# Optimization experiments

Measured on AMD Instinct MI355X. Metric: run time of the kernel, lower is better.

## Reference

```python
import jax, jax.numpy as jnp
import numpy as np

T = 200000


def _sine_layer(tvec, A, w, phi, phic, wc):
    # tvec: (t,), A/w/phi: (n,1), phic/wc: (1,)
    phi_static = jax.nn.relu(phic)  # (1,)
    w_static = jax.nn.relu(wc)
    ph = jax.nn.relu(phi) + phi_static  # (n,1)
    ww = jax.nn.relu(w) + w_static
    sine = A * jnp.sin(ww * tvec[None, :] + ph)  # (n,t)
    return sine, phi_static, w_static


def _selector_layer(tvec, wave_input, w, phi, phic, wc, phi_prev, w_prev):
    # wave_input: (n,t), w/phi: (m,n), phic/wc/phi_prev/w_prev: (1,)
    # NOTE: phi_prev/w_prev passed but phi_prev flag is False in the network,
    # so they are NOT added (matches torch: `if self.phi_prev and ...`).
    phi_static = jax.nn.relu(phic)
    w_static = jax.nn.relu(wc)
    ph = (jax.nn.relu(phi) + phi_static)[:, :, None]  # (m,n,1)
    ww = (jax.nn.relu(w) + w_static)[:, :, None]
    sine = 0.5 * jnp.sin(ww * tvec[None, None, :] + ph) + 0.5  # (m,n,t)
    out = jnp.einsum('mnt,nt->mt', sine, wave_input)  # (m,t)
    return out, phi_static, w_static


def setup_inputs() -> dict:
    key = jax.random.key(0)
    ks = jax.random.split(key, 18)
    r = lambda k, s: jax.random.normal(k, s, dtype=jnp.float32)
    return {
        'initial_wave_input': r(ks[0], (20, T)),
        'A0': r(ks[1], (20, 1)), 'w0': r(ks[2], (20, 1)), 'phi0': r(ks[3], (20, 1)),
        'wc0': r(ks[4], (1,)), 'phic0': r(ks[5], (1,)),
        'w1': r(ks[6], (25, 20)), 'phi1': r(ks[7], (25, 20)),
        'wc1': r(ks[8], (1,)), 'phic1': r(ks[9], (1,)),
        'w2': r(ks[10], (30, 25)), 'phi2': r(ks[11], (30, 25)),
        'wc2': r(ks[12], (1,)), 'phic2': r(ks[13], (1,)),
        'w3': r(ks[14], (1, 30)), 'phi3': r(ks[15], (1, 30)),
        'wc3': r(ks[16], (1,)), 'phic3': r(ks[17], (1,)),
    }


def reference(initial_wave_input, A0, w0, phi0, wc0, phic0,
              w1, phi1, wc1, phic1, w2, phi2, wc2, phic2,
              w3, phi3, wc3, phic3):
    tvec = jnp.linspace(1.0, 1000.0, T, dtype=jnp.float32)
    # initial_wave_input is an argument of the torch module but is never used.
    s, phi, w = _sine_layer(tvec, A0, w0, phi0, phic0, wc0)
    s, phi, w = _selector_layer(tvec, s, w1, phi1, phic1, wc1, phi, w)
    s, phi, w = _selector_layer(tvec, s, w2, phi2, phic2, wc2, phi, w)
    s, phi, w = _selector_layer(tvec, s, w3, phi3, phic3, wc3, phi, w)
    return s  # (1, t)
```

## Files before the change

### kernel.cpp

```cpp
#include <hip/hip_runtime.h>
#include <hip/hip_bf16.h>

#define T_TOTAL 200000

typedef float v4f __attribute__((ext_vector_type(4)));

__device__ float g_P[4496];

__device__ __forceinline__ float sinp(float rev) {
    float g = __builtin_amdgcn_fractf(rev);
    float h = g - 0.5f;
    float u = h * h;
    float p = fmaf(45.621248f, u, -82.391040f);
    p = fmaf(p, u, 64.671616f);
    p = fmaf(p, u, -19.730960f);
    p = fmaf(p, u, 0.9999618f);
    return p;
}

__global__ void prep_kernel(
    const float* __restrict__ A0,
    const float* __restrict__ w0, const float* __restrict__ phi0,
    const float* __restrict__ wc0, const float* __restrict__ phic0,
    const float* __restrict__ w1, const float* __restrict__ phi1,
    const float* __restrict__ wc1, const float* __restrict__ phic1,
    const float* __restrict__ w2, const float* __restrict__ phi2,
    const float* __restrict__ wc2, const float* __restrict__ phic2,
    const float* __restrict__ w3, const float* __restrict__ phi3,
    const float* __restrict__ wc3, const float* __restrict__ phic3)
{
    const int tid = blockIdx.x * blockDim.x + threadIdx.x;
    const int stride = blockDim.x * gridDim.x;

    const double I2PI = 0.15915494309189535;
    const double D64  = 64.0 * 999.0 / 199999.0;

    const double ws0 = fmax((double)wc0[0], 0.0), ps0 = fmax((double)phic0[0], 0.0);
    const double ws1 = fmax((double)wc1[0], 0.0), ps1 = fmax((double)phic1[0], 0.0);
    const double ws2 = fmax((double)wc2[0], 0.0), ps2 = fmax((double)phic2[0], 0.0);
    const double ws3 = fmax((double)wc3[0], 0.0), ps3 = fmax((double)phic3[0], 0.0);

    for (int n = tid; n < 20; n += stride) {
        double wr = fmax((double)w0[n], 0.0) + ws0;
        g_P[n]      = (float)(wr * I2PI);
        g_P[20 + n] = (float)((fmax((double)phi0[n], 0.0) + ps0) * I2PI + 0.25);
        g_P[40 + n] = (float)(2.0 * cos(wr * D64));
        g_P[60 + n] = A0[n];
    }
    for (int k = tid; k < 20 * 32; k += stride) {
        const int n = k >> 5, m = k & 31;
        float wwf = 0.0f, phf = 0.25f, cf = 2.0f;
        if (m < 25) {
            const int s = m * 20 + n;
            double wr = fmax((double)w1[s], 0.0) + ws1;
            wwf = (float)(wr * I2PI);
            phf = (float)((fmax((double)phi1[s], 0.0) + ps1) * I2PI + 0.25);
            cf  = (float)(2.0 * cos(wr * D64));
        }
        g_P[80 + 96 * n + m]      = wwf;
        g_P[80 + 96 * n + 32 + m] = phf;
        g_P[80 + 96 * n + 64 + m] = cf;
    }
    for (int k = tid; k < 25 * 32; k += stride) {
        const int n = k >> 5, m = k & 31;
        float wwf = 0.0f, phf = 0.25f, cf = 2.0f;
        if (m < 30) {
            const int s = m * 25 + n;
            double wr = fmax((double)w2[s], 0.0) + ws2;
            wwf = (float)(wr * I2PI);
            phf = (float)((fmax((double)phi2[s], 0.0) + ps2) * I2PI + 0.25);
            cf  = (float)(2.0 * cos(wr * D64));
        }
        g_P[2000 + 96 * n + m]      = wwf;
        g_P[2000 + 96 * n + 32 + m] = phf;
        g_P[2000 + 96 * n + 64 + m] = cf;
    }
    for (int k = tid; k < 32; k += stride) {
        float wwf = 0.0f, phf = 0.0f, cf = 2.0f;
        if (k < 30) {
            double wr = fmax((double)w3[k], 0.0) + ws3;
            wwf = (float)(wr * I2PI);
            phf = (float)((fmax((double)phi3[k], 0.0) + ps3) * I2PI + 0.25);
            cf  = (float)(2.0 * cos(wr * D64));
        }
        g_P[4400 + k]      = wwf;
        g_P[4400 + 32 + k] = phf;
        g_P[4400 + 64 + k] = cf;
    }
}

__launch_bounds__(256)
__global__ void wave_main(float* __restrict__ out)
{
    __shared__ float sh0[20][64][4];
    __shared__ float sh1[25][64][4];
    __shared__ float shp[4][64][4];

    const int l = threadIdx.x & 63;
    const int w = __builtin_amdgcn_readfirstlane(threadIdx.x >> 6);
    const int tb = blockIdx.x * 256;
    const float STEP = 999.0f / 199999.0f;

    float tv[4];
#pragma unroll
    for (int j = 0; j < 4; ++j)
        tv[j] = fmaf((float)(tb + l + 64 * j), STEP, 1.0f);

#pragma unroll
    for (int i = 0; i < 5; ++i) {
        const int n = 5 * w + i;
        const float ww = g_P[n], ph = g_P[20 + n], C = g_P[40 + n], A = g_P[60 + n];
        float x0 = A * sinp(fmaf(ww, tv[0], ph));
        float x1 = A * sinp(fmaf(ww, tv[1], ph));
        float x2 = fmaf(C, x1, -x0);
        float x3 = fmaf(C, x2, -x1);
        *(v4f*)&sh0[n][l][0] = (v4f){x0, x1, x2, x3};
    }
    __syncthreads();

    float acc1[8][4] = {};
    float sum0[4] = {0.f, 0.f, 0.f, 0.f};
#pragma clang loop unroll(disable)
    for (int n = 0; n < 20; ++n) {
        const v4f s0 = *(const v4f*)&sh0[n][l][0];
#pragma unroll
        for (int j = 0; j < 4; ++j) sum0[j] += s0[j];
        const float* __restrict__ pb = &g_P[80 + 96 * n + 8 * w];
#pragma unroll
        for (int k = 0; k < 8; ++k) {
            const float ww = pb[k], ph = pb[32 + k], C = pb[64 + k];
            float x0 = sinp(fmaf(ww, tv[0], ph));
            float x1 = sinp(fmaf(ww, tv[1], ph));
            float x2 = fmaf(C, x1, -x0);
            float x3 = fmaf(C, x2, -x1);
            acc1[k][0] = fmaf(x0, s0[0], acc1[k][0]);
            acc1[k][1] = fmaf(x1, s0[1], acc1[k][1]);
            acc1[k][2] = fmaf(x2, s0[2], acc1[k][2]);
            acc1[k][3] = fmaf(x3, s0[3], acc1[k][3]);
        }
    }
#pragma unroll
    for (int k = 0; k < 8; ++k) {
        if (8 * w + k < 25) {
            v4f v;
#pragma unroll
            for (int j = 0; j < 4; ++j) v[j] = fmaf(0.5f, acc1[k][j], 0.5f * sum0[j]);
            *(v4f*)&sh1[8 * w + k][l][0] = v;
        }
    }
    __syncthreads();

    float acc2[8][4] = {};
    float sum1[4] = {0.f, 0.f, 0.f, 0.f};
#pragma clang loop unroll(disable)
    for (int n = 0; n < 25; ++n) {
        const v4f s1 = *(const v4f*)&sh1[n][l][0];
#pragma unroll
        for (int j = 0; j < 4; ++j) sum1[j] += s1[j];
        const float* __restrict__ pb = &g_P[2000 + 96 * n + 8 * w];
#pragma unroll
        for (int k = 0; k < 8; ++k) {
            const float ww = pb[k], ph = pb[32 + k], C = pb[64 + k];
            float x0 = sinp(fmaf(ww, tv[0], ph));
            float x1 = sinp(fmaf(ww, tv[1], ph));
            float x2 = fmaf(C, x1, -x0);
            float x3 = fmaf(C, x2, -x1);
            acc2[k][0] = fmaf(x0, s1[0], acc2[k][0]);
            acc2[k][1] = fmaf(x1, s1[1], acc2[k][1]);
            acc2[k][2] = fmaf(x2, s1[2], acc2[k][2]);
            acc2[k][3] = fmaf(x3, s1[3], acc2[k][3]);
        }
    }
    float s2r[8][4];
#pragma unroll
    for (int k = 0; k < 8; ++k)
#pragma unroll
        for (int j = 0; j < 4; ++j)
            s2r[k][j] = fmaf(0.5f, acc2[k][j], 0.5f * sum1[j]);

    float pw[4] = {0.f, 0.f, 0.f, 0.f};
    {
        const float* __restrict__ pb = &g_P[4400 + 8 * w];
#pragma unroll
        for (int k = 0; k < 8; ++k) {
            if (8 * w + k < 30) {
                const float ww = pb[k], ph = pb[32 + k], C = pb[64 + k];
                float x0 = sinp(fmaf(ww, tv[0], ph));
                float x1 = sinp(fmaf(ww, tv[1], ph));
                float x2 = fmaf(C, x1, -x0);
                float x3 = fmaf(C, x2, -x1);
                pw[0] = fmaf(fmaf(0.5f, x0, 0.5f), s2r[k][0], pw[0]);
                pw[1] = fmaf(fmaf(0.5f, x1, 0.5f), s2r[k][1], pw[1]);
                pw[2] = fmaf(fmaf(0.5f, x2, 0.5f), s2r[k][2], pw[2]);
                pw[3] = fmaf(fmaf(0.5f, x3, 0.5f), s2r[k][3], pw[3]);
            }
        }
    }
    *(v4f*)&shp[w][l][0] = (v4f){pw[0], pw[1], pw[2], pw[3]};
    __syncthreads();

    const float r = (shp[0][l][w] + shp[1][l][w]) + (shp[2][l][w] + shp[3][l][w]);
    const int tt = tb + l + 64 * w;
    if (tt < T_TOTAL) out[tt] = r;
}

extern "C" void kernel_launch(void* const* d_in, const int* in_sizes, int n_in,
                              void* d_out, int out_size, void* d_ws, size_t ws_size,
                              hipStream_t stream) {
    (void)in_sizes; (void)n_in; (void)d_ws; (void)ws_size; (void)out_size;
    const float* A0    = (const float*)d_in[1];
    const float* w0    = (const float*)d_in[2];
    const float* phi0  = (const float*)d_in[3];
    const float* wc0   = (const float*)d_in[4];
    const float* phic0 = (const float*)d_in[5];
    const float* w1    = (const float*)d_in[6];
    const float* phi1  = (const float*)d_in[7];
    const float* wc1   = (const float*)d_in[8];
    const float* phic1 = (const float*)d_in[9];
    const float* w2    = (const float*)d_in[10];
    const float* phi2  = (const float*)d_in[11];
    const float* wc2   = (const float*)d_in[12];
    const float* phic2 = (const float*)d_in[13];
    const float* w3    = (const float*)d_in[14];
    const float* phi3  = (const float*)d_in[15];
    const float* wc3   = (const float*)d_in[16];
    const float* phic3 = (const float*)d_in[17];

    float* out = (float*)d_out;

    hipLaunchKernelGGL(prep_kernel, dim3(6), dim3(256), 0, stream,
                       A0, w0, phi0, wc0, phic0,
                       w1, phi1, wc1, phic1,
                       w2, phi2, wc2, phic2,
                       w3, phi3, wc3, phic3);

    const int grid = (T_TOTAL + 255) / 256;
    hipLaunchKernelGGL(wave_main, dim3(grid), dim3(256), 0, stream, out);
}
```

Before: 54.69 us.

## Split selector output channels across eight wavefronts per block instead of four

Doubles the block to 512 threads so each wavefront handles 4 output channels per selector layer instead of 8, while each block still covers 256 time points. The parameter table is padded to 24 layer-0 entries so each of the 8 waves computes 3 input waves. Shared memory is overlaid so the partial-sum buffer reuses the first buffer, which needs an extra barrier, and the final reduction sums 8 partials per point. The aim is to cut per-thread register pressure and serial work and so raise occupancy. The cost is that the shared s0/s1 loads and their running sums are now repeated across twice as many waves.

```diff
diff --git a/kernel.cpp b/kernel.cpp
--- a/kernel.cpp
+++ b/kernel.cpp
@@ -5,7 +5,7 @@
 
 typedef float v4f __attribute__((ext_vector_type(4)));
 
-__device__ float g_P[4496];
+__device__ float g_P[4512];
 
 __device__ __forceinline__ float sinp(float rev) {
     float g = __builtin_amdgcn_fractf(rev);
@@ -40,12 +40,19 @@
     const double ws2 = fmax((double)wc2[0], 0.0), ps2 = fmax((double)phic2[0], 0.0);
     const double ws3 = fmax((double)wc3[0], 0.0), ps3 = fmax((double)phic3[0], 0.0);
 
-    for (int n = tid; n < 20; n += stride) {
-        double wr = fmax((double)w0[n], 0.0) + ws0;
-        g_P[n]      = (float)(wr * I2PI);
-        g_P[20 + n] = (float)((fmax((double)phi0[n], 0.0) + ps0) * I2PI + 0.25);
-        g_P[40 + n] = (float)(2.0 * cos(wr * D64));
-        g_P[60 + n] = A0[n];
+    for (int n = tid; n < 24; n += stride) {
+        float wwf = 0.0f, phf = 0.25f, cf = 2.0f, af = 0.0f;
+        if (n < 20) {
+            double wr = fmax((double)w0[n], 0.0) + ws0;
+            wwf = (float)(wr * I2PI);
+            phf = (float)((fmax((double)phi0[n], 0.0) + ps0) * I2PI + 0.25);
+            cf  = (float)(2.0 * cos(wr * D64));
+            af  = A0[n];
+        }
+        g_P[n]      = wwf;
+        g_P[24 + n] = phf;
+        g_P[48 + n] = cf;
+        g_P[72 + n] = af;
     }
     for (int k = tid; k < 20 * 32; k += stride) {
         const int n = k >> 5, m = k & 31;
@@ -57,9 +64,9 @@
             phf = (float)((fmax((double)phi1[s], 0.0) + ps1) * I2PI + 0.25);
             cf  = (float)(2.0 * cos(wr * D64));
         }
-        g_P[80 + 96 * n + m]      = wwf;
-        g_P[80 + 96 * n + 32 + m] = phf;
-        g_P[80 + 96 * n + 64 + m] = cf;
+        g_P[96 + 96 * n + m]      = wwf;
+        g_P[96 + 96 * n + 32 + m] = phf;
+        g_P[96 + 96 * n + 64 + m] = cf;
     }
     for (int k = tid; k < 25 * 32; k += stride) {
         const int n = k >> 5, m = k & 31;
@@ -71,30 +78,31 @@
             phf = (float)((fmax((double)phi2[s], 0.0) + ps2) * I2PI + 0.25);
             cf  = (float)(2.0 * cos(wr * D64));
         }
-        g_P[2000 + 96 * n + m]      = wwf;
-        g_P[2000 + 96 * n + 32 + m] = phf;
-        g_P[2000 + 96 * n + 64 + m] = cf;
+        g_P[2016 + 96 * n + m]      = wwf;
+        g_P[2016 + 96 * n + 32 + m] = phf;
+        g_P[2016 + 96 * n + 64 + m] = cf;
     }
     for (int k = tid; k < 32; k += stride) {
-        float wwf = 0.0f, phf = 0.0f, cf = 2.0f;
+        float wwf = 0.0f, phf = 0.25f, cf = 2.0f;
         if (k < 30) {
             double wr = fmax((double)w3[k], 0.0) + ws3;
             wwf = (float)(wr * I2PI);
             phf = (float)((fmax((double)phi3[k], 0.0) + ps3) * I2PI + 0.25);
             cf  = (float)(2.0 * cos(wr * D64));
         }
-        g_P[4400 + k]      = wwf;
-        g_P[4400 + 32 + k] = phf;
-        g_P[4400 + 64 + k] = cf;
-    }
-}
-
-__launch_bounds__(256)
+        g_P[4416 + k]      = wwf;
+        g_P[4416 + 32 + k] = phf;
+        g_P[4416 + 64 + k] = cf;
+    }
+}
+
+__launch_bounds__(512)
 __global__ void wave_main(float* __restrict__ out)
 {
-    __shared__ float sh0[20][64][4];
-    __shared__ float sh1[25][64][4];
-    __shared__ float shp[4][64][4];
+    __shared__ float smem[12544];
+    float* const sh0 = smem;
+    float* const sh1 = smem + 6144;
+    float* const shp = smem;
 
     const int l = threadIdx.x & 63;
     const int w = __builtin_amdgcn_readfirstlane(threadIdx.x >> 6);
@@ -107,27 +115,27 @@
         tv[j] = fmaf((float)(tb + l + 64 * j), STEP, 1.0f);
 
 #pragma unroll
-    for (int i = 0; i < 5; ++i) {
-        const int n = 5 * w + i;
-        const float ww = g_P[n], ph = g_P[20 + n], C = g_P[40 + n], A = g_P[60 + n];
+    for (int i = 0; i < 3; ++i) {
+        const int n = 3 * w + i;
+        const float ww = g_P[n], ph = g_P[24 + n], C = g_P[48 + n], A = g_P[72 + n];
         float x0 = A * sinp(fmaf(ww, tv[0], ph));
         float x1 = A * sinp(fmaf(ww, tv[1], ph));
         float x2 = fmaf(C, x1, -x0);
         float x3 = fmaf(C, x2, -x1);
-        *(v4f*)&sh0[n][l][0] = (v4f){x0, x1, x2, x3};
-    }
-    __syncthreads();
-
-    float acc1[8][4] = {};
+        *(v4f*)&sh0[n * 256 + l * 4] = (v4f){x0, x1, x2, x3};
+    }
+    __syncthreads();
+
+    float acc1[4][4] = {};
     float sum0[4] = {0.f, 0.f, 0.f, 0.f};
 #pragma clang loop unroll(disable)
     for (int n = 0; n < 20; ++n) {
-        const v4f s0 = *(const v4f*)&sh0[n][l][0];
+        const v4f s0 = *(const v4f*)&sh0[n * 256 + l * 4];
 #pragma unroll
         for (int j = 0; j < 4; ++j) sum0[j] += s0[j];
-        const float* __restrict__ pb = &g_P[80 + 96 * n + 8 * w];
-#pragma unroll
-        for (int k = 0; k < 8; ++k) {
+        const float* __restrict__ pb = &g_P[96 + 96 * n + 4 * w];
+#pragma unroll
+        for (int k = 0; k < 4; ++k) {
             const float ww = pb[k], ph = pb[32 + k], C = pb[64 + k];
             float x0 = sinp(fmaf(ww, tv[0], ph));
             float x1 = sinp(fmaf(ww, tv[1], ph));
@@ -140,26 +148,26 @@
         }
     }
 #pragma unroll
-    for (int k = 0; k < 8; ++k) {
-        if (8 * w + k < 25) {
+    for (int k = 0; k < 4; ++k) {
+        if (4 * w + k < 25) {
             v4f v;
 #pragma unroll
             for (int j = 0; j < 4; ++j) v[j] = fmaf(0.5f, acc1[k][j], 0.5f * sum0[j]);
-            *(v4f*)&sh1[8 * w + k][l][0] = v;
-        }
-    }
-    __syncthreads();
-
-    float acc2[8][4] = {};
+            *(v4f*)&sh1[(4 * w + k) * 256 + l * 4] = v;
+        }
+    }
+    __syncthreads();
+
+    float acc2[4][4] = {};
     float sum1[4] = {0.f, 0.f, 0.f, 0.f};
 #pragma clang loop unroll(disable)
     for (int n = 0; n < 25; ++n) {
-        const v4f s1 = *(const v4f*)&sh1[n][l][0];
+        const v4f s1 = *(const v4f*)&sh1[n * 256 + l * 4];
 #pragma unroll
         for (int j = 0; j < 4; ++j) sum1[j] += s1[j];
-        const float* __restrict__ pb = &g_P[2000 + 96 * n + 8 * w];
-#pragma unroll
-        for (int k = 0; k < 8; ++k) {
+        const float* __restrict__ pb = &g_P[2016 + 96 * n + 4 * w];
+#pragma unroll
+        for (int k = 0; k < 4; ++k) {
             const float ww = pb[k], ph = pb[32 + k], C = pb[64 + k];
             float x0 = sinp(fmaf(ww, tv[0], ph));
             float x1 = sinp(fmaf(ww, tv[1], ph));
@@ -171,19 +179,19 @@
             acc2[k][3] = fmaf(x3, s1[3], acc2[k][3]);
         }
     }
-    float s2r[8][4];
-#pragma unroll
-    for (int k = 0; k < 8; ++k)
+    float s2r[4][4];
+#pragma unroll
+    for (int k = 0; k < 4; ++k)
 #pragma unroll
         for (int j = 0; j < 4; ++j)
             s2r[k][j] = fmaf(0.5f, acc2[k][j], 0.5f * sum1[j]);
 
     float pw[4] = {0.f, 0.f, 0.f, 0.f};
     {
-        const float* __restrict__ pb = &g_P[4400 + 8 * w];
-#pragma unroll
-        for (int k = 0; k < 8; ++k) {
-            if (8 * w + k < 30) {
+        const float* __restrict__ pb = &g_P[4416 + 4 * w];
+#pragma unroll
+        for (int k = 0; k < 4; ++k) {
+            if (4 * w + k < 30) {
                 const float ww = pb[k], ph = pb[32 + k], C = pb[64 + k];
                 float x0 = sinp(fmaf(ww, tv[0], ph));
                 float x1 = sinp(fmaf(ww, tv[1], ph));
@@ -196,12 +204,18 @@
             }
         }
     }
-    *(v4f*)&shp[w][l][0] = (v4f){pw[0], pw[1], pw[2], pw[3]};
-    __syncthreads();
-
-    const float r = (shp[0][l][w] + shp[1][l][w]) + (shp[2][l][w] + shp[3][l][w]);
-    const int tt = tb + l + 64 * w;
-    if (tt < T_TOTAL) out[tt] = r;
+    __syncthreads();
+    *(v4f*)&shp[w * 256 + l * 4] = (v4f){pw[0], pw[1], pw[2], pw[3]};
+    __syncthreads();
+
+    if (w < 4) {
+        float r = 0.0f;
+#pragma unroll
+        for (int w2 = 0; w2 < 8; ++w2)
+            r += shp[w2 * 256 + l * 4 + w];
+        const int tt = tb + l + 64 * w;
+        if (tt < T_TOTAL) out[tt] = r;
+    }
 }
 
 extern "C" void kernel_launch(void* const* d_in, const int* in_sizes, int n_in,
@@ -235,5 +249,5 @@
                        w3, phi3, wc3, phic3);
 
     const int grid = (T_TOTAL + 255) / 256;
-    hipLaunchKernelGGL(wave_main, dim3(grid), dim3(256), 0, stream, out);
-}
+    hipLaunchKernelGGL(wave_main, dim3(grid), dim3(512), 0, stream, out);
+}
```

New measurement: 52.12 us. 4.7% less time.
